# Kernel tuning notes

Hardware: AMD Instinct MI355X
Metric: run time of the kernel (lower is better)

The kernel has to match this reference:

```python
import jax, jax.numpy as jnp
import numpy as np

K = 20
EPS = 1e-5
NEG_SLOPE = 0.2


def setup_inputs() -> dict:
    key = jax.random.key(0)
    k1, k2, k3, k4 = jax.random.split(key, 4)
    B, C, N, O = 8, 64, 4096, 64
    x = jax.random.normal(k1, (B, C, N), dtype=jnp.float32)
    # Conv2d(2C, O, kernel_size=1, bias=False) -> weight [O, 2C]
    W = jax.random.normal(k2, (O, 2 * C), dtype=jnp.float32) * (1.0 / np.sqrt(2 * C))
    gamma = jnp.ones((O,), dtype=jnp.float32)
    beta = jnp.zeros((O,), dtype=jnp.float32)
    return {"x": x, "W": W, "gamma": gamma, "beta": beta}


def reference(x, W, gamma, beta):
    B, C, N = x.shape
    xt = jnp.transpose(x, (0, 2, 1))  # [B, N, C]
    # knn: negative squared pairwise distance, topk -> nearest neighbors
    inner = jnp.einsum('bic,bjc->bij', xt, xt)  # [B, N, N]
    xx = jnp.sum(xt * xt, axis=-1)              # [B, N]
    neg_dist = 2.0 * inner - xx[:, :, None] - xx[:, None, :]
    _, idx = jax.lax.top_k(neg_dist, K)         # [B, N, K]
    # gather neighbor features: [B, N, K, C]
    feature = jax.vmap(lambda f, i: f[i])(xt, idx)
    x_central = jnp.broadcast_to(xt[:, :, None, :], (B, N, K, C))
    edge = jnp.concatenate([feature - x_central, x_central], axis=-1)  # [B, N, K, 2C]
    # 1x1 conv == matmul over channel dim
    y = jnp.einsum('bnkc,oc->bnko', edge, W)    # [B, N, K, O]
    # BatchNorm2d in training mode: batch stats over (B, N, K) per channel
    mean = jnp.mean(y, axis=(0, 1, 2))
    var = jnp.var(y, axis=(0, 1, 2))
    y = (y - mean) * jax.lax.rsqrt(var + EPS) * gamma + beta
    y = jnp.where(y >= 0, y, NEG_SLOPE * y)     # LeakyReLU(0.2)
    out = jnp.max(y, axis=2)                    # max over k neighbors -> [B, N, O]
    return jnp.transpose(out, (0, 2, 1))        # [B, O, N]
```

## Files before the change

### kernel.cpp

```cpp
#include <hip/hip_runtime.h>
#include <cstdint>
#include <cstddef>

#define BB 8
#define CC 64
#define NN 4096
#define OO 64
#define KK 20
#define TWO_C 128
#define BN (BB * NN)

#define JCH 128
#define GSPLIT 8
#define GJPB (NN / GSPLIT)
#define CSPLIT 4
#define CJPB (NN / CSPLIT)
#define SEGCAP 32

typedef float vf4 __attribute__((ext_vector_type(4)));
typedef float f4  __attribute__((ext_vector_type(4)));
typedef _Float16 hf2 __attribute__((ext_vector_type(2)));
typedef _Float16 h8  __attribute__((ext_vector_type(8)));

__device__ __forceinline__ unsigned int pack_h2(float a, float b) {
    hf2 h; h.x = (_Float16)a; h.y = (_Float16)b;
    return __builtin_bit_cast(unsigned int, h);
}

__device__ __forceinline__ unsigned int fmap(float d) {
    unsigned int s = __float_as_uint(d);
    return s ^ (unsigned int)(((int)s >> 31) | 0x80000000);
}

__global__ __launch_bounds__(256) void transpose_kernel(const float* __restrict__ x,
                                                        float* __restrict__ xT,
                                                        unsigned int* __restrict__ xTh) {
    __shared__ float t[64][65];
    const int b = blockIdx.y;
    const int n0 = blockIdx.x * 64;
    const int tid = threadIdx.x;
    const int ln = tid & 63, g = tid >> 6;
#pragma unroll
    for (int i = 0; i < 16; ++i) {
        int c = g * 16 + i;
        t[c][ln] = x[((size_t)b * CC + c) * NN + n0 + ln];
    }
    __syncthreads();
#pragma unroll
    for (int i = 0; i < 16; ++i) {
        int nl = g * 16 + i;
        xT[((size_t)b * NN + n0 + nl) * CC + ln] = t[ln][nl];
    }
#pragma unroll
    for (int it = 0; it < 8; ++it) {
        int e = it * 256 + tid;
        int nl = e >> 5, cp = e & 31;
        xTh[((size_t)b * NN + n0 + nl) * 32 + cp] = pack_h2(t[2*cp][nl], t[2*cp+1][nl]);
    }
}

__global__ __launch_bounds__(256) void xx_kernel(const float* __restrict__ x,
                                                 float* __restrict__ xx) {
    int t = blockIdx.x * 256 + threadIdx.x;
    int b = t >> 12, n = t & (NN - 1);
    const float* xp = x + (size_t)b * CC * NN + n;
    float acc = 0.f;
#pragma unroll
    for (int c = 0; c < CC; ++c) {
        float v = xp[(size_t)c * NN];
        acc += v * v;
    }
    xx[t] = acc;
}

__global__ __launch_bounds__(256) void knn_gmax_kernel(const unsigned int* __restrict__ xTh,
                                                       const float* __restrict__ xx,
                                                       float* __restrict__ gmaxG) {
    __shared__ unsigned int stage[JCH * 36];
    __shared__ float xxh[JCH];
    const int tid = threadIdx.x;
    const int wv = tid >> 6, lane = tid & 63;
    const int lcol = lane & 15, lrow = lane >> 4;
    const int b = blockIdx.z;
    const int i0 = blockIdx.x * 128;
    const int j0 = blockIdx.y * GJPB;
    const unsigned int* xb = xTh + (size_t)b * NN * 32;
    const float* xxb = xx + (size_t)b * NN;

    const uint4* ap0 = (const uint4*)(xb + (size_t)(i0 + wv * 32 + lcol) * 32 + lrow * 4);
    const uint4* ap1 = (const uint4*)(xb + (size_t)(i0 + wv * 32 + 16 + lcol) * 32 + lrow * 4);
    uint4 A00 = ap0[0], A01 = ap0[4];
    uint4 A10 = ap1[0], A11 = ap1[4];

    float m[8];
#pragma unroll
    for (int s = 0; s < 8; ++s) m[s] = -3.4e38f;

    uint4 pf[4];
    float pxx;
    {
        const uint4* src = (const uint4*)(xb + (size_t)j0 * 32);
#pragma unroll
        for (int gi = 0; gi < 4; ++gi) pf[gi] = src[gi * 256 + tid];
        pxx = xxb[j0 + (tid & 127)];
    }

    int g = j0 >> 7;
    for (int jc = j0; jc < j0 + GJPB; jc += JCH) {
        __syncthreads();
#pragma unroll
        for (int gi = 0; gi < 4; ++gi) {
            int e4 = gi * 256 + tid;
            *(uint4*)&stage[(e4 >> 3) * 36 + (e4 & 7) * 4] = pf[gi];
        }
        if (tid < JCH) xxh[tid] = 0.5f * pxx;
        __syncthreads();
        if (jc + JCH < j0 + GJPB) {
            const uint4* src = (const uint4*)(xb + (size_t)(jc + JCH) * 32);
#pragma unroll
            for (int gi = 0; gi < 4; ++gi) pf[gi] = src[gi * 256 + tid];
            pxx = xxb[jc + JCH + (tid & 127)];
        }
#pragma unroll
        for (int jt = 0; jt < 8; ++jt) {
            const uint4* bp = (const uint4*)&stage[(jt * 16 + lcol) * 36 + lrow * 4];
            uint4 B0 = bp[0], B1 = bp[4];
            f4 acc0 = {0.f, 0.f, 0.f, 0.f};
            f4 acc1 = {0.f, 0.f, 0.f, 0.f};
            acc0 = __builtin_amdgcn_mfma_f32_16x16x32_f16(__builtin_bit_cast(h8, A00), __builtin_bit_cast(h8, B0), acc0, 0, 0, 0);
            acc0 = __builtin_amdgcn_mfma_f32_16x16x32_f16(__builtin_bit_cast(h8, A01), __builtin_bit_cast(h8, B1), acc0, 0, 0, 0);
            acc1 = __builtin_amdgcn_mfma_f32_16x16x32_f16(__builtin_bit_cast(h8, A10), __builtin_bit_cast(h8, B0), acc1, 0, 0, 0);
            acc1 = __builtin_amdgcn_mfma_f32_16x16x32_f16(__builtin_bit_cast(h8, A11), __builtin_bit_cast(h8, B1), acc1, 0, 0, 0);
            float h = xxh[jt * 16 + lcol];
#pragma unroll
            for (int r = 0; r < 4; ++r) {
                m[r]     = fmaxf(m[r],     acc0[r] - h);
                m[4 + r] = fmaxf(m[4 + r], acc1[r] - h);
            }
        }
#pragma unroll
        for (int s = 0; s < 8; ++s) {
#pragma unroll
            for (int off = 1; off < 16; off <<= 1)
                m[s] = fmaxf(m[s], __shfl_xor(m[s], off));
        }
        if (lcol == 0) {
            int r0 = b * NN + i0 + wv * 32 + lrow * 4;
            f4 m0; m0[0] = m[0]; m0[1] = m[1]; m0[2] = m[2]; m0[3] = m[3];
            f4 m1; m1[0] = m[4]; m1[1] = m[5]; m1[2] = m[6]; m1[3] = m[7];
            *(f4*)&gmaxG[(size_t)g * BN + r0]      = m0;
            *(f4*)&gmaxG[(size_t)g * BN + r0 + 16] = m1;
        }
#pragma unroll
        for (int s = 0; s < 8; ++s) m[s] = -3.4e38f;
        ++g;
    }
}

__global__ __launch_bounds__(256) void knn_thresh_kernel(const float* __restrict__ gmaxG,
                                                         float* __restrict__ Tg) {
    const int row = blockIdx.x * 256 + threadIdx.x;
    float L[KK];
#pragma unroll
    for (int s = 0; s < KK; ++s) L[s] = -3.4e38f;
#pragma unroll
    for (int g = 0; g < 32; ++g) {
        float xv = gmaxG[(size_t)g * BN + row];
#pragma unroll
        for (int s = 0; s < KK; ++s) {
            float hi = fmaxf(xv, L[s]);
            xv = fminf(xv, L[s]);
            L[s] = hi;
        }
    }
    Tg[row] = L[KK - 1];
}

__global__ __launch_bounds__(256) void knn_collect_kernel(const unsigned int* __restrict__ xTh,
                                                          const float* __restrict__ xx,
                                                          const float* __restrict__ Tg,
                                                          unsigned short* __restrict__ cand,
                                                          unsigned int* __restrict__ cntS) {
    __shared__ unsigned int stage[JCH * 36];
    __shared__ float xxh[JCH];
    __shared__ unsigned short bufL[128][SEGCAP];
    __shared__ unsigned int cntL[128];
    const int tid = threadIdx.x;
    const int wv = tid >> 6, lane = tid & 63;
    const int lcol = lane & 15, lrow = lane >> 4;
    const int b = blockIdx.z;
    const int i0 = blockIdx.x * 128;
    const int seg = blockIdx.y;
    const int j0 = seg * CJPB;
    const unsigned int* xb = xTh + (size_t)b * NN * 32;
    const float* xxb = xx + (size_t)b * NN;

    if (tid < 128) cntL[tid] = 0;

    const uint4* ap0 = (const uint4*)(xb + (size_t)(i0 + wv * 32 + lcol) * 32 + lrow * 4);
    const uint4* ap1 = (const uint4*)(xb + (size_t)(i0 + wv * 32 + 16 + lcol) * 32 + lrow * 4);
    uint4 A00 = ap0[0], A01 = ap0[4];
    uint4 A10 = ap1[0], A11 = ap1[4];

    const int rl0 = wv * 32 + lrow * 4;
    const int gr0 = b * NN + i0 + rl0;
    f4 t0 = *(const f4*)&Tg[gr0];
    f4 t1 = *(const f4*)&Tg[gr0 + 16];

    uint4 pf[4];
    float pxx;
    {
        const uint4* src = (const uint4*)(xb + (size_t)j0 * 32);
#pragma unroll
        for (int gi = 0; gi < 4; ++gi) pf[gi] = src[gi * 256 + tid];
        pxx = xxb[j0 + (tid & 127)];
    }

    for (int jc = j0; jc < j0 + CJPB; jc += JCH) {
        __syncthreads();
#pragma unroll
        for (int gi = 0; gi < 4; ++gi) {
            int e4 = gi * 256 + tid;
            *(uint4*)&stage[(e4 >> 3) * 36 + (e4 & 7) * 4] = pf[gi];
        }
        if (tid < JCH) xxh[tid] = 0.5f * pxx;
        __syncthreads();
        if (jc + JCH < j0 + CJPB) {
            const uint4* src = (const uint4*)(xb + (size_t)(jc + JCH) * 32);
#pragma unroll
            for (int gi = 0; gi < 4; ++gi) pf[gi] = src[gi * 256 + tid];
            pxx = xxb[jc + JCH + (tid & 127)];
        }
#pragma unroll
        for (int jt = 0; jt < 8; ++jt) {
            const uint4* bp = (const uint4*)&stage[(jt * 16 + lcol) * 36 + lrow * 4];
            uint4 B0 = bp[0], B1 = bp[4];
            f4 acc0 = {0.f, 0.f, 0.f, 0.f};
            f4 acc1 = {0.f, 0.f, 0.f, 0.f};
            acc0 = __builtin_amdgcn_mfma_f32_16x16x32_f16(__builtin_bit_cast(h8, A00), __builtin_bit_cast(h8, B0), acc0, 0, 0, 0);
            acc0 = __builtin_amdgcn_mfma_f32_16x16x32_f16(__builtin_bit_cast(h8, A01), __builtin_bit_cast(h8, B1), acc0, 0, 0, 0);
            acc1 = __builtin_amdgcn_mfma_f32_16x16x32_f16(__builtin_bit_cast(h8, A10), __builtin_bit_cast(h8, B0), acc1, 0, 0, 0);
            acc1 = __builtin_amdgcn_mfma_f32_16x16x32_f16(__builtin_bit_cast(h8, A11), __builtin_bit_cast(h8, B1), acc1, 0, 0, 0);
            float h = xxh[jt * 16 + lcol];
            const int jj = jc + jt * 16 + lcol;
#pragma unroll
            for (int r = 0; r < 4; ++r) {
                if (acc0[r] - h >= t0[r]) {
                    unsigned int s = atomicAdd(&cntL[rl0 + r], 1u);
                    if (s < SEGCAP) bufL[rl0 + r][s] = (unsigned short)jj;
                }
                if (acc1[r] - h >= t1[r]) {
                    unsigned int s = atomicAdd(&cntL[rl0 + 16 + r], 1u);
                    if (s < SEGCAP) bufL[rl0 + 16 + r][s] = (unsigned short)jj;
                }
            }
        }
    }
    __syncthreads();
    const unsigned int* bl = (const unsigned int*)&bufL[0][0];
    unsigned int* cd = (unsigned int*)(cand + ((size_t)seg * BN + b * NN + i0) * SEGCAP);
#pragma unroll
    for (int e = tid; e < 128 * SEGCAP / 2; e += 256) cd[e] = bl[e];
    if (tid < 128) cntS[(size_t)seg * BN + b * NN + i0 + tid] = cntL[tid];
}

__global__ __launch_bounds__(256, 3) void knn_merge_kernel(const float* __restrict__ xT,
                                                           const float* __restrict__ xx,
                                                           const unsigned short* __restrict__ cand,
                                                           const unsigned int* __restrict__ cntS,
                                                           unsigned short* __restrict__ idx_out) {
    __shared__ unsigned long long shk[64][4][KK + 1];
    const int tid = threadIdx.x;
    const int sub = tid & 3, rloc = tid >> 2;
    const int r = blockIdx.x * 64 + rloc;
    const int b = r >> 12, i = r & (NN - 1);
    const float* xTb = xT + (size_t)b * NN * CC;
    const float* xxb = xx + b * NN;

    vf4 xiv[CC / 4];
    const float* xip = xTb + (size_t)i * CC;
#pragma unroll
    for (int c4 = 0; c4 < CC / 4; ++c4) {
        const float* p = xip + 4 * c4;
        asm volatile("global_load_dwordx4 %0, %1, off" : "=v"(xiv[c4]) : "v"(p));
    }
    asm volatile("s_waitcnt vmcnt(0)" ::: "memory");

    unsigned long long Lk[KK];
#pragma unroll
    for (int s = 0; s < KK; ++s) Lk[s] = 0ull;

    bool ovf = false;
    unsigned int myc = 0;
#pragma unroll
    for (int s2 = 0; s2 < CSPLIT; ++s2) {
        unsigned int c2 = cntS[(size_t)s2 * BN + r];
        ovf |= (c2 > SEGCAP);
        if (s2 == sub) myc = c2;
    }
    const unsigned short* cp = cand + ((size_t)sub * BN + r) * SEGCAP;
    const int lim = ovf ? (NN / 4) : (int)myc;
    for (int q = 0; q < lim; ++q) {
        const int jj = ovf ? (sub + 4 * q) : (int)cp[q];
        const float* xj = xTb + (size_t)jj * CC;
        float a0 = 0.f, a1 = 0.f, a2 = 0.f, a3 = 0.f;
#pragma unroll
        for (int c4 = 0; c4 < CC / 4; ++c4) {
            a0 = fmaf(xiv[c4].x, xj[4 * c4 + 0], a0);
            a1 = fmaf(xiv[c4].y, xj[4 * c4 + 1], a1);
            a2 = fmaf(xiv[c4].z, xj[4 * c4 + 2], a2);
            a3 = fmaf(xiv[c4].w, xj[4 * c4 + 3], a3);
        }
        float d = 2.f * ((a0 + a1) + (a2 + a3)) - xxb[jj];
        unsigned long long ku = ((unsigned long long)fmap(d) << 32) | (unsigned int)(NN - 1 - jj);
#pragma unroll
        for (int s = 0; s < KK; ++s) {
            bool take = ku > Lk[s];
            unsigned long long hi = take ? ku : Lk[s];
            ku = take ? Lk[s] : ku;
            Lk[s] = hi;
        }
    }

#pragma unroll
    for (int s = 0; s < KK; ++s) shk[rloc][sub][s] = Lk[s];
    shk[rloc][sub][KK] = 0ull;
    __builtin_amdgcn_wave_barrier();

    if (sub == 0) {
        int h0 = 0, h1 = 0, h2 = 0, h3 = 0;
        unsigned short* op = idx_out + (size_t)r * KK;
        for (int k = 0; k < KK; ++k) {
            unsigned long long k0 = shk[rloc][0][h0];
            unsigned long long k1 = shk[rloc][1][h1];
            unsigned long long k2 = shk[rloc][2][h2];
            unsigned long long k3 = shk[rloc][3][h3];
            unsigned long long best = k0; int src = 0;
            if (k1 > best) { best = k1; src = 1; }
            if (k2 > best) { best = k2; src = 2; }
            if (k3 > best) { best = k3; src = 3; }
            op[k] = (unsigned short)(NN - 1 - (unsigned int)(best & 0xFFFFFFFFull));
            h0 += (src == 0); h1 += (src == 1); h2 += (src == 2); h3 += (src == 3);
        }
    }
}

__global__ __launch_bounds__(256) void pd_kernel(const float* __restrict__ x,
                                                 const float* __restrict__ W,
                                                 float* __restrict__ P,
                                                 float* __restrict__ Dd) {
    __shared__ float w1T[CC][32];
    __shared__ float wdT[CC][32];
    const int tid = threadIdx.x;
    const int b = blockIdx.y;
    const int o0 = blockIdx.z * 32;
    for (int e = tid; e < 32 * CC; e += 256) {
        int ol = e >> 6, c = e & 63;
        float w1 = W[(o0 + ol) * TWO_C + c];
        float w2 = W[(o0 + ol) * TWO_C + CC + c];
        w1T[c][ol] = w1;
        wdT[c][ol] = w2 - w1;
    }
    __syncthreads();
    const int n = blockIdx.x * 256 + tid;
    float accp[32], accd[32];
#pragma unroll
    for (int i = 0; i < 32; ++i) { accp[i] = 0.f; accd[i] = 0.f; }
    const float* xp = x + (size_t)b * CC * NN + n;
    for (int c = 0; c < CC; ++c) {
        float xv = xp[(size_t)c * NN];
        const float4* w1r = (const float4*)&w1T[c][0];
        const float4* wdr = (const float4*)&wdT[c][0];
#pragma unroll
        for (int g = 0; g < 8; ++g) {
            float4 aw = w1r[g]; float4 bw = wdr[g];
            accp[4*g+0] += xv * aw.x; accp[4*g+1] += xv * aw.y;
            accp[4*g+2] += xv * aw.z; accp[4*g+3] += xv * aw.w;
            accd[4*g+0] += xv * bw.x; accd[4*g+1] += xv * bw.y;
            accd[4*g+2] += xv * bw.z; accd[4*g+3] += xv * bw.w;
        }
    }
    size_t base = ((size_t)b * NN + n) * OO + o0;
#pragma unroll
    for (int g = 0; g < 8; ++g) {
        *(float4*)&P[base + 4*g]  = make_float4(accp[4*g], accp[4*g+1], accp[4*g+2], accp[4*g+3]);
        *(float4*)&Dd[base + 4*g] = make_float4(accd[4*g], accd[4*g+1], accd[4*g+2], accd[4*g+3]);
    }
}

__global__ __launch_bounds__(256) void stats_kernel(const float* __restrict__ P,
                                                    const float* __restrict__ Dd,
                                                    const unsigned short* __restrict__ idx,
                                                    double* __restrict__ partials) {
    const int tid = threadIdx.x;
    const int o = tid & 63, g = tid >> 6;
    const int row0 = blockIdx.x * 32;
    double s1 = 0.0, s2 = 0.0;
    for (int i = 0; i < 8; ++i) {
        int row = row0 + g + 4 * i;
        int b = row >> 12;
        float d = Dd[(size_t)row * OO + o];
        const unsigned short* ip = idx + (size_t)row * KK;
        const float* Pb = P + ((size_t)b * NN) * OO;
#pragma unroll
        for (int k = 0; k < KK; ++k) {
            int j = ip[k];
            float y = Pb[(size_t)j * OO + o] + d;
            s1 += (double)y;
            s2 += (double)y * (double)y;
        }
    }
    __shared__ double r1[4][64];
    __shared__ double r2[4][64];
    r1[g][o] = s1; r2[g][o] = s2;
    __syncthreads();
    if (g == 0) {
        double a1 = r1[0][o] + r1[1][o] + r1[2][o] + r1[3][o];
        double a2 = r2[0][o] + r2[1][o] + r2[2][o] + r2[3][o];
        partials[(size_t)blockIdx.x * 128 + o]      = a1;
        partials[(size_t)blockIdx.x * 128 + 64 + o] = a2;
    }
}

#define NSTATB (BB * NN / 32)
__global__ void finalize_kernel(const double* __restrict__ partials,
                                const float* __restrict__ gamma,
                                const float* __restrict__ beta,
                                float* __restrict__ ss) {
    int o = threadIdx.x;
    double s1 = 0.0, s2 = 0.0;
    for (int blk = 0; blk < NSTATB; ++blk) {
        s1 += partials[(size_t)blk * 128 + o];
        s2 += partials[(size_t)blk * 128 + 64 + o];
    }
    const double cnt = (double)BB * NN * KK;
    double mean = s1 / cnt;
    double var = s2 / cnt - mean * mean;
    double rs = 1.0 / sqrt(var + 1e-5);
    double sc = (double)gamma[o] * rs;
    ss[o] = (float)sc;
    ss[64 + o] = (float)((double)beta[o] - mean * sc);
}

__global__ __launch_bounds__(256) void out_kernel(const float* __restrict__ P,
                                                  const float* __restrict__ Dd,
                                                  const unsigned short* __restrict__ idx,
                                                  const float* __restrict__ ss,
                                                  float* __restrict__ out) {
    __shared__ float tile[32][65];
    const int tid = threadIdx.x;
    const int o = tid & 63, g = tid >> 6;
    const int b = blockIdx.y;
    const int n0 = blockIdx.x * 32;
    const float sc = ss[o], sh = ss[64 + o];
    const float* Pb = P + ((size_t)b * NN) * OO;
    for (int i = 0; i < 8; ++i) {
        int nl = g + 4 * i;
        int row = b * NN + n0 + nl;
        float d = Dd[(size_t)row * OO + o];
        const unsigned short* ip = idx + (size_t)row * KK;
        float mv = -__builtin_inff();
#pragma unroll
        for (int k = 0; k < KK; ++k) {
            int j = ip[k];
            float y = Pb[(size_t)j * OO + o] + d;
            float t = y * sc + sh;
            t = (t >= 0.f) ? t : 0.2f * t;
            mv = fmaxf(mv, t);
        }
        tile[nl][o] = mv;
    }
    __syncthreads();
    const int nn = tid & 31, og = tid >> 5;
    for (int i = 0; i < 8; ++i) {
        int oo = og + 8 * i;
        out[((size_t)b * OO + oo) * NN + n0 + nn] = tile[nn][oo];
    }
}

extern "C" void kernel_launch(void* const* d_in, const int* in_sizes, int n_in,
                              void* d_out, int out_size, void* d_ws, size_t ws_size,
                              hipStream_t stream) {
    (void)in_sizes; (void)n_in; (void)out_size; (void)ws_size;
    const float* x     = (const float*)d_in[0];
    const float* W     = (const float*)d_in[1];
    const float* gamma = (const float*)d_in[2];
    const float* beta  = (const float*)d_in[3];
    float* out = (float*)d_out;

    char* ws = (char*)d_ws;
    float*          xx       = (float*)ws;
    float*          xT       = (float*)(ws + 131072);
    unsigned int*   xTh      = (unsigned int*)(ws + 8519680);
    float*          gmaxG    = (float*)(ws + 12713984);
    unsigned short* cand     = (unsigned short*)(ws + 12713984);
    float*          Tg       = (float*)(ws + 21102592);
    unsigned int*   cntS     = (unsigned int*)(ws + 21233664);
    unsigned short* idx      = (unsigned short*)(ws + 8519680);
    float*          P        = (float*)(ws + 131072);
    float*          Dd       = (float*)(ws + 12713984);
    double*         partials = (double*)(ws + 21102592);
    float*          ss       = (float*)(ws + 22151168);

    transpose_kernel<<<dim3(NN / 64, BB), 256, 0, stream>>>(x, xT, xTh);
    xx_kernel<<<dim3(BB * NN / 256), 256, 0, stream>>>(x, xx);
    knn_gmax_kernel<<<dim3(NN / 128, GSPLIT, BB), 256, 0, stream>>>(xTh, xx, gmaxG);
    knn_thresh_kernel<<<dim3(BN / 256), 256, 0, stream>>>(gmaxG, Tg);
    knn_collect_kernel<<<dim3(NN / 128, CSPLIT, BB), 256, 0, stream>>>(xTh, xx, Tg, cand, cntS);
    knn_merge_kernel<<<dim3(BN / 64), 256, 0, stream>>>(xT, xx, cand, cntS, idx);
    pd_kernel<<<dim3(NN / 256, BB, 2), 256, 0, stream>>>(x, W, P, Dd);
    stats_kernel<<<dim3(BN / 32), 256, 0, stream>>>(P, Dd, idx, partials);
    finalize_kernel<<<1, 64, 0, stream>>>(partials, gamma, beta, ss);
    out_kernel<<<dim3(NN / 32, BB), 256, 0, stream>>>(P, Dd, idx, ss, out);
}
```

Before: 371.6 us.

## Rewrite kNN merge as one-wave-per-row bitonic sort over candidates

```diff
diff --git a/kernel.cpp b/kernel.cpp
--- a/kernel.cpp
+++ b/kernel.cpp
@@ -30,6 +30,13 @@
 __device__ __forceinline__ unsigned int fmap(float d) {
     unsigned int s = __float_as_uint(d);
     return s ^ (unsigned int)(((int)s >> 31) | 0x80000000);
+}
+
+__device__ __forceinline__ unsigned long long cmpx(unsigned long long key, int lane, int j, bool dirDesc) {
+    unsigned long long o = __shfl_xor(key, j, 64);
+    bool lower = (lane & j) == 0;
+    bool takeMax = (dirDesc == lower);
+    return ((o > key) == takeMax) ? o : key;
 }
 
 __global__ __launch_bounds__(256) void transpose_kernel(const float* __restrict__ x,
@@ -264,85 +271,111 @@
     if (tid < 128) cntS[(size_t)seg * BN + b * NN + i0 + tid] = cntL[tid];
 }
 
-__global__ __launch_bounds__(256, 3) void knn_merge_kernel(const float* __restrict__ xT,
-                                                           const float* __restrict__ xx,
-                                                           const unsigned short* __restrict__ cand,
-                                                           const unsigned int* __restrict__ cntS,
-                                                           unsigned short* __restrict__ idx_out) {
-    __shared__ unsigned long long shk[64][4][KK + 1];
-    const int tid = threadIdx.x;
-    const int sub = tid & 3, rloc = tid >> 2;
-    const int r = blockIdx.x * 64 + rloc;
-    const int b = r >> 12, i = r & (NN - 1);
+__global__ __launch_bounds__(256) void knn_merge_kernel(const float* __restrict__ xT,
+                                                        const float* __restrict__ xx,
+                                                        const unsigned short* __restrict__ cand,
+                                                        const unsigned int* __restrict__ cntS,
+                                                        unsigned short* __restrict__ idx_out) {
+    const int tid = threadIdx.x;
+    const int wv = tid >> 6, lane = tid & 63;
+    const int rr = __builtin_amdgcn_readfirstlane(blockIdx.x * 4 + wv);
+    const int b = rr >> 12, i = rr & (NN - 1);
     const float* xTb = xT + (size_t)b * NN * CC;
     const float* xxb = xx + b * NN;
 
     vf4 xiv[CC / 4];
     const float* xip = xTb + (size_t)i * CC;
 #pragma unroll
-    for (int c4 = 0; c4 < CC / 4; ++c4) {
-        const float* p = xip + 4 * c4;
-        asm volatile("global_load_dwordx4 %0, %1, off" : "=v"(xiv[c4]) : "v"(p));
-    }
-    asm volatile("s_waitcnt vmcnt(0)" ::: "memory");
-
-    unsigned long long Lk[KK];
-#pragma unroll
-    for (int s = 0; s < KK; ++s) Lk[s] = 0ull;
-
-    bool ovf = false;
-    unsigned int myc = 0;
-#pragma unroll
-    for (int s2 = 0; s2 < CSPLIT; ++s2) {
-        unsigned int c2 = cntS[(size_t)s2 * BN + r];
-        ovf |= (c2 > SEGCAP);
-        if (s2 == sub) myc = c2;
-    }
-    const unsigned short* cp = cand + ((size_t)sub * BN + r) * SEGCAP;
-    const int lim = ovf ? (NN / 4) : (int)myc;
-    for (int q = 0; q < lim; ++q) {
-        const int jj = ovf ? (sub + 4 * q) : (int)cp[q];
+    for (int c4 = 0; c4 < CC / 4; ++c4) xiv[c4] = *(const vf4*)(xip + 4 * c4);
+
+    const unsigned int c0 = cntS[(size_t)0 * BN + rr];
+    const unsigned int c1 = cntS[(size_t)1 * BN + rr];
+    const unsigned int c2 = cntS[(size_t)2 * BN + rr];
+    const unsigned int c3 = cntS[(size_t)3 * BN + rr];
+    const bool segovf = (c0 > SEGCAP) || (c1 > SEGCAP) || (c2 > SEGCAP) || (c3 > SEGCAP);
+    const unsigned int p1 = c0, p2 = c0 + c1, p3 = c0 + c1 + c2, total = p3 + c3;
+
+    auto dot_key = [&](int jj) -> unsigned long long {
         const float* xj = xTb + (size_t)jj * CC;
         float a0 = 0.f, a1 = 0.f, a2 = 0.f, a3 = 0.f;
 #pragma unroll
         for (int c4 = 0; c4 < CC / 4; ++c4) {
-            a0 = fmaf(xiv[c4].x, xj[4 * c4 + 0], a0);
-            a1 = fmaf(xiv[c4].y, xj[4 * c4 + 1], a1);
-            a2 = fmaf(xiv[c4].z, xj[4 * c4 + 2], a2);
-            a3 = fmaf(xiv[c4].w, xj[4 * c4 + 3], a3);
+            vf4 xjv = *(const vf4*)(xj + 4 * c4);
+            a0 = fmaf(xiv[c4].x, xjv.x, a0);
+            a1 = fmaf(xiv[c4].y, xjv.y, a1);
+            a2 = fmaf(xiv[c4].z, xjv.z, a2);
+            a3 = fmaf(xiv[c4].w, xjv.w, a3);
         }
         float d = 2.f * ((a0 + a1) + (a2 + a3)) - xxb[jj];
-        unsigned long long ku = ((unsigned long long)fmap(d) << 32) | (unsigned int)(NN - 1 - jj);
-#pragma unroll
-        for (int s = 0; s < KK; ++s) {
-            bool take = ku > Lk[s];
-            unsigned long long hi = take ? ku : Lk[s];
-            ku = take ? Lk[s] : ku;
-            Lk[s] = hi;
-        }
-    }
-
-#pragma unroll
-    for (int s = 0; s < KK; ++s) shk[rloc][sub][s] = Lk[s];
-    shk[rloc][sub][KK] = 0ull;
-    __builtin_amdgcn_wave_barrier();
-
-    if (sub == 0) {
-        int h0 = 0, h1 = 0, h2 = 0, h3 = 0;
-        unsigned short* op = idx_out + (size_t)r * KK;
-        for (int k = 0; k < KK; ++k) {
-            unsigned long long k0 = shk[rloc][0][h0];
-            unsigned long long k1 = shk[rloc][1][h1];
-            unsigned long long k2 = shk[rloc][2][h2];
-            unsigned long long k3 = shk[rloc][3][h3];
-            unsigned long long best = k0; int src = 0;
-            if (k1 > best) { best = k1; src = 1; }
-            if (k2 > best) { best = k2; src = 2; }
-            if (k3 > best) { best = k3; src = 3; }
-            op[k] = (unsigned short)(NN - 1 - (unsigned int)(best & 0xFFFFFFFFull));
-            h0 += (src == 0); h1 += (src == 1); h2 += (src == 2); h3 += (src == 3);
-        }
-    }
+        return ((unsigned long long)fmap(d) << 32) | (unsigned int)(NN - 1 - jj);
+    };
+
+    auto fetch_key = [&](unsigned int l) -> unsigned long long {
+        if (l >= total) return 0ull;
+        int jj;
+        if (l < p1)      jj = cand[((size_t)0 * BN + rr) * SEGCAP + l];
+        else if (l < p2) jj = cand[((size_t)1 * BN + rr) * SEGCAP + (l - p1)];
+        else if (l < p3) jj = cand[((size_t)2 * BN + rr) * SEGCAP + (l - p2)];
+        else             jj = cand[((size_t)3 * BN + rr) * SEGCAP + (l - p3)];
+        return dot_key(jj);
+    };
+
+    unsigned long long kout;
+    if (!segovf && total <= 64) {
+        unsigned long long key = fetch_key((unsigned int)lane);
+#pragma unroll
+        for (int k = 2; k <= 64; k <<= 1) {
+            bool dir = (lane & k) == 0;
+#pragma unroll
+            for (int j = k >> 1; j > 0; j >>= 1) key = cmpx(key, lane, j, dir);
+        }
+        kout = key;
+    } else if (!segovf) {
+        unsigned long long key  = fetch_key((unsigned int)lane);
+        unsigned long long key2 = fetch_key((unsigned int)lane + 64);
+#pragma unroll
+        for (int k = 2; k <= 64; k <<= 1) {
+            bool dir0 = (lane & k) == 0;
+            bool dir1 = (k == 64) ? false : dir0;
+#pragma unroll
+            for (int j = k >> 1; j > 0; j >>= 1) {
+                key  = cmpx(key,  lane, j, dir0);
+                key2 = cmpx(key2, lane, j, dir1);
+            }
+        }
+        {
+            unsigned long long mx = key2 > key ? key2 : key;
+            unsigned long long mn = key2 > key ? key : key2;
+            key = mx; key2 = mn;
+        }
+#pragma unroll
+        for (int j = 32; j > 0; j >>= 1) {
+            key  = cmpx(key,  lane, j, true);
+            key2 = cmpx(key2, lane, j, true);
+        }
+        kout = key;
+    } else {
+        unsigned long long run = 0ull;
+        for (int t = 0; t < NN / 64; ++t) {
+            unsigned long long key = dot_key(t * 64 + lane);
+#pragma unroll
+            for (int k = 2; k <= 64; k <<= 1) {
+                bool dir = (lane & k) == 0;
+#pragma unroll
+                for (int j = k >> 1; j > 0; j >>= 1) key = cmpx(key, lane, j, dir);
+            }
+            unsigned long long rev = __shfl(run, 63 - lane, 64);
+            key = key > rev ? key : rev;
+#pragma unroll
+            for (int j = 32; j > 0; j >>= 1) key = cmpx(key, lane, j, true);
+            run = key;
+        }
+        kout = run;
+    }
+
+    if (lane < KK)
+        idx_out[(size_t)rr * KK + lane] =
+            (unsigned short)(NN - 1 - (unsigned int)(kout & 0xFFFFFFFFull));
 }
 
 __global__ __launch_bounds__(256) void pd_kernel(const float* __restrict__ x,
@@ -507,7 +540,7 @@
     knn_gmax_kernel<<<dim3(NN / 128, GSPLIT, BB), 256, 0, stream>>>(xTh, xx, gmaxG);
     knn_thresh_kernel<<<dim3(BN / 256), 256, 0, stream>>>(gmaxG, Tg);
     knn_collect_kernel<<<dim3(NN / 128, CSPLIT, BB), 256, 0, stream>>>(xTh, xx, Tg, cand, cntS);
-    knn_merge_kernel<<<dim3(BN / 64), 256, 0, stream>>>(xT, xx, cand, cntS, idx);
+    knn_merge_kernel<<<dim3(BN / 4), 256, 0, stream>>>(xT, xx, cand, cntS, idx);
     pd_kernel<<<dim3(NN / 256, BB, 2), 256, 0, stream>>>(x, W, P, Dd);
     stats_kernel<<<dim3(BN / 32), 256, 0, stream>>>(P, Dd, idx, partials);
     finalize_kernel<<<1, 64, 0, stream>>>(partials, gamma, beta, ss);
```

Measured after the change: 344.1 us. 1.08x faster.
